# Kernel optimization log

Hardware: AMD Instinct MI355X
Metric: run time of the kernel (lower is better)

The kernel has to match this reference:

```python
import jax, jax.numpy as jnp
import numpy as np

B, S, E, H, D = 4, 2048, 1024, 16, 64  # batch, seq, embed, heads, head_dim


def setup_inputs() -> dict:
    key = jax.random.key(0)
    k1, k2, k3 = jax.random.split(key, 3)
    x = jax.random.normal(k1, (B, S, E), dtype=jnp.float32)
    qkv_w = jax.random.normal(k2, (E, H, 3 * D), dtype=jnp.float32) * (1.0 / np.sqrt(E))
    qkv_b = jnp.zeros((H, 3 * D), dtype=jnp.float32)
    out_w = jax.random.normal(k3, (H, D, E), dtype=jnp.float32) * (1.0 / np.sqrt(H * D))
    out_b = jnp.zeros((E,), dtype=jnp.float32)
    return {"x": x, "qkv_w": qkv_w, "qkv_b": qkv_b, "out_w": out_w, "out_b": out_b}


def _large_negative_number(dtype):
    return jnp.asarray(-0.7 * jnp.finfo(dtype).max, dtype=dtype)


def reference(x, qkv_w, qkv_b, out_w, out_b):
    # qkv projection: LinearGeneral(E -> (H, 3D))
    qkv = jnp.einsum('bse,ehd->bshd', x, qkv_w) + qkv_b  # [B,S,H,3D]
    q, k, v = jnp.split(qkv, 3, axis=-1)  # each [B,S,H,D]
    logits = jnp.einsum('bqhd,bkhd->bhqk', q, k)  # [B,H,S,S]
    logits = logits / jnp.sqrt(jnp.asarray(q.shape[-1], logits.dtype))
    mask = jnp.tril(jnp.ones((q.shape[1], q.shape[1]), dtype=jnp.bool_))
    logits = jnp.where(mask, logits, _large_negative_number(logits.dtype))
    probs = jax.nn.softmax(logits, axis=-1)
    attn = jnp.einsum('bhqk,bkhd->bqhd', probs, v)  # [B,S,H,D]
    # output projection: LinearGeneral((H, D) -> E)
    return jnp.einsum('bqhd,hde->bqe', attn, out_w) + out_b
```

## Files before the change

kernel.cpp:

```cpp
#include <hip/hip_runtime.h>

typedef unsigned int u32;
typedef _Float16 f16;
typedef _Float16 f16x8 __attribute__((ext_vector_type(8)));
typedef _Float16 f16x4 __attribute__((ext_vector_type(4)));
typedef float f32x4 __attribute__((ext_vector_type(4)));

#define LOG2E 1.4426950408889634f

__device__ __forceinline__ void gl_lds16(const void* g, void* l) {
  __builtin_amdgcn_global_load_lds(
      (const __attribute__((address_space(1))) u32*)g,
      (__attribute__((address_space(3))) u32*)l, 16, 0, 0);
}

__device__ __forceinline__ f32x4 mfma16(f16x8 a, f16x8 b, f32x4 c) {
  return __builtin_amdgcn_mfma_f32_16x16x32_f16(a, b, c, 0, 0, 0);
}

__global__ void k_cvt(const float* __restrict__ in, f16* __restrict__ out, int n8) {
  int stride = gridDim.x * blockDim.x;
  for (int i = blockIdx.x * blockDim.x + threadIdx.x; i < n8; i += stride) {
    f32x4 a = *(const f32x4*)(in + (size_t)i * 8);
    f32x4 b = *(const f32x4*)(in + (size_t)i * 8 + 4);
    f16x8 o;
    o[0] = (f16)a[0]; o[1] = (f16)a[1]; o[2] = (f16)a[2]; o[3] = (f16)a[3];
    o[4] = (f16)b[0]; o[5] = (f16)b[1]; o[6] = (f16)b[2]; o[7] = (f16)b[3];
    *(f16x8*)(out + (size_t)i * 8) = o;
  }
}

__global__ void k_tconv(const float* __restrict__ in, f16* __restrict__ out, int R, int C) {
  __shared__ f16 tile[32][33];
  int c0 = blockIdx.x * 32, r0 = blockIdx.y * 32;
  int tx = threadIdx.x, ty = threadIdx.y;
#pragma unroll
  for (int i = ty; i < 32; i += 8)
    tile[i][tx] = (f16)in[(size_t)(r0 + i) * C + c0 + tx];
  __syncthreads();
#pragma unroll
  for (int i = ty; i < 32; i += 8)
    out[(size_t)(c0 + i) * R + r0 + tx] = tile[tx][i];
}

__device__ __forceinline__ void gemm97(
    const f16* __restrict__ A, const f16* __restrict__ Bt,
    int bm, int bn, f16* SM, int w, int lane, f32x4 (&acc)[4][4]) {
  constexpr int KT = 32;
  const int g = lane >> 4, rl = lane & 15;
  const int l4 = lane >> 2, ls = lane & 3;
  const int sslot = ls ^ ((l4 >> 1) & 3);
  const int wr = w >> 1, wc = w & 1;

  const f16* aS = A + (size_t)(bm + w * 16 + l4) * 1024 + sslot * 8;
  const f16* bS = Bt + (size_t)(bn + w * 16 + l4) * 1024 + sslot * 8;

#define STG97(b, kt) do { \
    gl_lds16(aS + (kt) * 32,          SM + (b) * 8192 + w * 512); \
    gl_lds16(aS + 65536 + (kt) * 32,  SM + (b) * 8192 + 2048 + w * 512); \
    gl_lds16(bS + (kt) * 32,          SM + (b) * 8192 + 4096 + w * 512); \
    gl_lds16(bS + 65536 + (kt) * 32,  SM + (b) * 8192 + 6144 + w * 512); } while (0)

  const int ro = rl * 32 + ((g ^ ((rl >> 1) & 3)) * 8);

  STG97(0, 0);
  __syncthreads();

#pragma unroll 1
  for (int kt = 0; kt < KT; ++kt) {
    const int cur = kt & 1;
    if (kt + 1 < KT) STG97(cur ^ 1, kt + 1);
    const f16* SMb = SM + cur * 8192;
    f16x8 af[4], bf[4];
#pragma unroll
    for (int mi = 0; mi < 4; ++mi)
      af[mi] = *(const f16x8*)(SMb + wr * 2048 + mi * 512 + ro);
#pragma unroll
    for (int j = 0; j < 4; ++j)
      bf[j] = *(const f16x8*)(SMb + 4096 + wc * 2048 + j * 512 + ro);
    __builtin_amdgcn_s_setprio(1);
#pragma unroll
    for (int mi = 0; mi < 4; ++mi)
#pragma unroll
      for (int j = 0; j < 4; ++j)
        acc[mi][j] = mfma16(af[mi], bf[j], acc[mi][j]);
    __builtin_amdgcn_s_setprio(0);
    __syncthreads();
  }
#undef STG97
}

__global__ __launch_bounds__(256, 3) void k_gemm_qkv5(
    const f16* __restrict__ A, const f16* __restrict__ Bt,
    const float* __restrict__ bias,
    f16* __restrict__ qo, f16* __restrict__ ko2, f16* __restrict__ vto) {
  __shared__ __align__(16) f16 SM[16384];
  const int lin0 = blockIdx.y * 24 + blockIdx.x;
  const int lin = (lin0 & 7) * 192 + (lin0 >> 3);
  const int bn = (lin % 24) * 128, bm = (lin / 24) * 128;
  const int t = threadIdx.x, lane = t & 63, w = t >> 6;
  const int g = lane >> 4, rl = lane & 15;
  const int wr = w >> 1, wc = w & 1;

  f32x4 acc[4][4] = {};
  gemm97(A, Bt, bm, bn, SM, w, lane, acc);

#pragma unroll
  for (int i = 0; i < 4; ++i)
#pragma unroll
    for (int j = 0; j < 4; ++j)
#pragma unroll
      for (int r = 0; r < 4; ++r) {
        int m = bm + wr * 64 + i * 16 + g * 4 + r;
        int n = bn + wc * 64 + j * 16 + rl;
        float v = acc[i][j][r] + bias[n];
        int b = m >> 11, s = m & 2047;
        int h = n / 192, rem = n - h * 192;
        int tsel = rem >> 6, dd = rem & 63;
        size_t bh = (size_t)(b * 16 + h);
        if (tsel == 0)      qo[(bh * 2048 + s) * 64 + dd] = (f16)(v * (0.125f * LOG2E));
        else if (tsel == 1) ko2[(bh * 2048 + s) * 64 + dd] = (f16)v;
        else                vto[(bh * 64 + dd) * 2048 + s] = (f16)v;
      }
}

__global__ __launch_bounds__(256, 3) void k_gemm_out5(
    const f16* __restrict__ A, const f16* __restrict__ Bt,
    const float* __restrict__ bias, float* __restrict__ out) {
  __shared__ __align__(16) f16 SM[16384];
  const int lin0 = blockIdx.y * 8 + blockIdx.x;
  const int lin = (lin0 & 7) * 64 + (lin0 >> 3);
  const int bn = (lin % 8) * 128, bm = (lin / 8) * 128;
  const int t = threadIdx.x, lane = t & 63, w = t >> 6;
  const int g = lane >> 4, rl = lane & 15;
  const int wr = w >> 1, wc = w & 1;

  f32x4 acc[4][4] = {};
  gemm97(A, Bt, bm, bn, SM, w, lane, acc);

#pragma unroll
  for (int i = 0; i < 4; ++i)
#pragma unroll
    for (int j = 0; j < 4; ++j)
#pragma unroll
      for (int r = 0; r < 4; ++r) {
        int m = bm + wr * 64 + i * 16 + g * 4 + r;
        int n = bn + wc * 64 + j * 16 + rl;
        out[(size_t)m * 1024 + n] = acc[i][j][r] + bias[n];
      }
}

__global__ __launch_bounds__(256, 4) void k_attn5(
    const f16* __restrict__ q, const f16* __restrict__ kgl,
    const f16* __restrict__ vt, f16* __restrict__ o) {
  constexpr int S = 2048;
  __shared__ __align__(16) f16 Ks[2][64 * 64];
  __shared__ __align__(16) f16 Vs[2][64 * 64];
  __shared__ __align__(16) f16 Ps[4][16 * 64];

  const int d = blockIdx.x;
  const int bh = (d & 7) * 8 + ((d >> 3) & 7);
  const int v_ = d >> 6, g2 = v_ >> 2, r2 = v_ & 3;
  const int qb = (g2 == 0) ? 15 - r2 : (g2 == 1) ? r2 : (g2 == 2) ? 11 - r2 : 4 + r2;

  const int t = threadIdx.x, lane = t & 63, w = t >> 6;
  const int g = lane >> 4, rl = lane & 15;

  const f16* qp = q + ((size_t)bh * S + qb * 128) * 64;
  const f16* kb = kgl + (size_t)bh * S * 64;
  const f16* vb = vt + (size_t)bh * 64 * S;

  f16x8 qf[2][2];
#pragma unroll
  for (int sub = 0; sub < 2; ++sub)
#pragma unroll
    for (int ks = 0; ks < 2; ++ks)
      qf[sub][ks] = *(const f16x8*)(qp + (size_t)(w * 32 + sub * 16 + rl) * 64 + ks * 32 + g * 8);

  f32x4 oacc[2][4] = {};
  float lrow[2] = {0.f, 0.f};

  const int srow = lane >> 3;
  const int sslot = (lane & 7) ^ srow;

  const int nkt = 2 * qb + 2;
  const int qsub0 = qb * 128 + w * 32;
  const int qmaxw = qsub0 + 31;

  auto STAGE = [&](int bufi, int kt) {
#pragma unroll
    for (int i = 0; i < 2; ++i) {
      const int r0 = w * 16 + i * 8;
      gl_lds16(kb + (size_t)(kt * 64 + r0 + srow) * 64 + sslot * 8, &Ks[bufi][r0 * 64]);
      gl_lds16(vb + (size_t)(r0 + srow) * S + kt * 64 + sslot * 8, &Vs[bufi][r0 * 64]);
    }
  };

  STAGE(0, 0);
  __syncthreads();
  int buf = 0;

  for (int kt = 0; kt < nkt; ++kt) {
    if (kt + 1 < nkt) STAGE(buf ^ 1, kt + 1);

    if (kt * 64 <= qmaxw) {
      const f16* Kb = &Ks[buf][0];
      const f16* Vb = &Vs[buf][0];

      f32x4 sT[2][4] = {};
#pragma unroll
      for (int j = 0; j < 4; ++j)
#pragma unroll
        for (int ks = 0; ks < 2; ++ks) {
          int row = j * 16 + rl;
          f16x8 kf = *(const f16x8*)(Kb + row * 64 + (((ks * 4 + g) ^ (rl & 7)) * 8));
          sT[0][j] = mfma16(kf, qf[0][ks], sT[0][j]);
          sT[1][j] = mfma16(kf, qf[1][ks], sT[1][j]);
        }

      if (kt * 64 + 63 > qsub0) {
#pragma unroll
        for (int sub = 0; sub < 2; ++sub) {
          const int qs = qsub0 + sub * 16;
#pragma unroll
          for (int j = 0; j < 4; ++j)
#pragma unroll
            for (int r = 0; r < 4; ++r)
              if (kt * 64 + j * 16 + g * 4 + r > qs + rl) sT[sub][j][r] = -1e30f;
        }
      }

#pragma unroll
      for (int sub = 0; sub < 2; ++sub) {
        const int qsub = qsub0 + sub * 16;
        if (kt * 64 > qsub + 15) continue;

        float ps = 0.f;
#pragma unroll
        for (int j = 0; j < 4; ++j) {
          f16x4 pb;
#pragma unroll
          for (int r = 0; r < 4; ++r) {
            float pp = exp2f(sT[sub][j][r]);
            ps += pp;
            pb[r] = (f16)pp;
          }
          *(f16x4*)(&Ps[w][0] + rl * 64 + (((j * 2 + (g >> 1)) ^ (rl & 7)) * 8) + (g & 1) * 4) = pb;
        }
        lrow[sub] += ps;

        asm volatile("s_waitcnt lgkmcnt(0)" ::: "memory");
        __builtin_amdgcn_sched_barrier(0);

        f16x8 pf[2];
#pragma unroll
        for (int ks = 0; ks < 2; ++ks)
          pf[ks] = *(const f16x8*)(&Ps[w][0] + rl * 64 + (((ks * 4 + g) ^ (rl & 7)) * 8));

#pragma unroll
        for (int dj = 0; dj < 4; ++dj)
#pragma unroll
          for (int ks = 0; ks < 2; ++ks) {
            int vrow = dj * 16 + rl;
            f16x8 vf = *(const f16x8*)(Vb + vrow * 64 + (((ks * 4 + g) ^ (rl & 7)) * 8));
            oacc[sub][dj] = mfma16(pf[ks], vf, oacc[sub][dj]);
          }
      }
    }
    __syncthreads();
    buf ^= 1;
  }

  float rinv[2];
#pragma unroll
  for (int sub = 0; sub < 2; ++sub) {
    float s_ = lrow[sub];
    s_ += __shfl_xor(s_, 16, 64);
    s_ += __shfl_xor(s_, 32, 64);
    rinv[sub] = 1.0f / s_;
  }

  const int h = bh & 15;
  const size_t rowb = (size_t)(bh >> 4) * 2048 + qb * 128 + w * 32;
#pragma unroll
  for (int sub = 0; sub < 2; ++sub)
#pragma unroll
    for (int r = 0; r < 4; ++r) {
      float ri = __shfl(rinv[sub], g * 4 + r, 64);
#pragma unroll
      for (int dj = 0; dj < 4; ++dj)
        o[(rowb + sub * 16 + g * 4 + r) * 1024 + h * 64 + dj * 16 + rl] =
            (f16)(oacc[sub][dj][r] * ri);
    }
}

extern "C" void kernel_launch(void* const* d_in, const int* in_sizes, int n_in,
                              void* d_out, int out_size, void* d_ws, size_t ws_size,
                              hipStream_t stream) {
  (void)in_sizes; (void)n_in; (void)out_size; (void)ws_size;
  const float* x    = (const float*)d_in[0];
  const float* wqkv = (const float*)d_in[1];
  const float* bqkv = (const float*)d_in[2];
  const float* wo   = (const float*)d_in[3];
  const float* bo   = (const float*)d_in[4];
  float* out = (float*)d_out;
  char* ws = (char*)d_ws;

  f16* xb    = (f16*)(ws + 0);
  f16* wqkvt = (f16*)(ws + 16777216);
  f16* wot   = (f16*)(ws + 23068672);
  f16* qws   = (f16*)(ws + 25165824);
  f16* kws   = (f16*)(ws + 41943040);
  f16* vtws  = (f16*)(ws + 58720256);
  f16* attnb = xb;

  k_cvt<<<1024, 256, 0, stream>>>(x, xb, 8388608 / 8);
  k_tconv<<<dim3(96, 32), dim3(32, 8), 0, stream>>>(wqkv, wqkvt, 1024, 3072);
  k_tconv<<<dim3(32, 32), dim3(32, 8), 0, stream>>>(wo, wot, 1024, 1024);
  k_gemm_qkv5<<<dim3(24, 64), 256, 0, stream>>>(xb, wqkvt, bqkv, qws, kws, vtws);
  k_attn5<<<1024, 256, 0, stream>>>(qws, kws, vtws, attnb);
  k_gemm_out5<<<dim3(8, 64), 256, 0, stream>>>(attnb, wot, bo, out);
}
```

Baseline: 187.0 us.

## Use 128x256 triple-buffered QKV GEMM and restructure attention softmax/PV loop

Replaces the QKV projection GEMM with a 128x256 tile kernel. Each wave owns a 64-column slab with eight M fragments, fed by a three-stage LDS ring of async global-to-LDS loads with explicit waitcnt and barriers. In attention, the P·V MFMAs for both 16-row sub-tiles are merged into one loop that shares each V fragment load. MFMA sections run at raised wave priority, and exp results are packed with cvt_pkrtz. This trades higher LDS and register use (two blocks per CU instead of three) for more reuse per tile, and it drops the per-subtile causal skip in attention, which adds some wasted work on fully masked rows.

After: 184.1 us. Within noise of the previous version (-1.5%).

```diff
diff --git a/kernel.cpp b/kernel.cpp
--- a/kernel.cpp
+++ b/kernel.cpp
@@ -5,6 +5,7 @@
 typedef _Float16 f16x8 __attribute__((ext_vector_type(8)));
 typedef _Float16 f16x4 __attribute__((ext_vector_type(4)));
 typedef float f32x4 __attribute__((ext_vector_type(4)));
+typedef _Float16 __attribute__((address_space(3))) lf16;
 
 #define LOG2E 1.4426950408889634f
 
@@ -16,6 +17,12 @@
 
 __device__ __forceinline__ f32x4 mfma16(f16x8 a, f16x8 b, f32x4 c) {
   return __builtin_amdgcn_mfma_f32_16x16x32_f16(a, b, c, 0, 0, 0);
+}
+
+__device__ __forceinline__ f16x8 ldsr(const f16* p) {
+  f16x8 r;
+  asm volatile("ds_read_b128 %0, %1" : "=v"(r) : "v"((const lf16*)p));
+  return r;
 }
 
 __global__ void k_cvt(const float* __restrict__ in, f16* __restrict__ out, int n8) {
@@ -43,6 +50,124 @@
     out[(size_t)(c0 + i) * R + r0 + tx] = tile[tx][i];
 }
 
+__device__ __forceinline__ void gemm_fatA(
+    const f16* __restrict__ A, const f16* __restrict__ Bt,
+    int bm, int bn, f16* SM, int w, int lane, f32x4 (&acc)[8][4]) {
+  constexpr int KT = 32;
+  const int g = lane >> 4, rl = lane & 15;
+  const int l4 = lane >> 2, ls = lane & 3;
+  const int sslot = ls ^ ((l4 >> 1) & 3);
+
+  const f16* aS = A + (size_t)(bm + w * 32 + l4) * 1024 + sslot * 8;
+  const f16* bS = Bt + (size_t)(bn + w * 16 + l4) * 1024 + sslot * 8;
+  f16* aD = SM + w * 1024;
+  f16* bD = SM + 4096 + w * 512;
+
+#define ASTG0(b, kt) do { \
+    gl_lds16(aS + (kt) * 32,          aD + (b) * 12288); \
+    gl_lds16(aS + 16384 + (kt) * 32,  aD + (b) * 12288 + 512); \
+    gl_lds16(bS + (kt) * 32,          bD + (b) * 12288); } while (0)
+#define ASTG1(b, kt) do { \
+    gl_lds16(bS + 65536 + (kt) * 32,  bD + (b) * 12288 + 2048); \
+    gl_lds16(bS + 131072 + (kt) * 32, bD + (b) * 12288 + 4096); \
+    gl_lds16(bS + 196608 + (kt) * 32, bD + (b) * 12288 + 6144); } while (0)
+
+  ASTG0(0, 0); ASTG1(0, 0);
+  ASTG0(1, 1); ASTG1(1, 1);
+  asm volatile("s_waitcnt vmcnt(6)" ::: "memory");
+  __builtin_amdgcn_s_barrier();
+
+  const int ro = rl * 32 + ((g ^ ((rl >> 1) & 3)) * 8);
+
+  int c = 0, cs = 2;
+#pragma unroll 1
+  for (int kt = 0; kt < KT; ++kt) {
+    const f16* SMc = SM + c * 12288;
+    const bool stg = (kt + 2 < KT);
+    f16x8 bf[4], af[4];
+
+    {
+#pragma unroll
+      for (int j = 0; j < 4; ++j)
+        bf[j] = ldsr(SMc + 4096 + w * 2048 + j * 512 + ro);
+#pragma unroll
+      for (int mi = 0; mi < 4; ++mi)
+        af[mi] = ldsr(SMc + mi * 512 + ro);
+      if (stg) ASTG0(cs, kt + 2);
+      __builtin_amdgcn_s_barrier();
+      asm volatile("s_waitcnt lgkmcnt(0)");
+      __builtin_amdgcn_sched_barrier(0);
+      __builtin_amdgcn_s_setprio(1);
+#pragma unroll
+      for (int mi = 0; mi < 4; ++mi)
+#pragma unroll
+        for (int j = 0; j < 4; ++j)
+          acc[mi][j] = mfma16(af[mi], bf[j], acc[mi][j]);
+      __builtin_amdgcn_s_setprio(0);
+      __builtin_amdgcn_sched_barrier(0);
+      __builtin_amdgcn_s_barrier();
+    }
+    {
+#pragma unroll
+      for (int mi = 0; mi < 4; ++mi)
+        af[mi] = ldsr(SMc + (4 + mi) * 512 + ro);
+      if (stg) ASTG1(cs, kt + 2);
+      __builtin_amdgcn_s_barrier();
+      asm volatile("s_waitcnt lgkmcnt(0)");
+      __builtin_amdgcn_sched_barrier(0);
+      __builtin_amdgcn_s_setprio(1);
+#pragma unroll
+      for (int mi = 0; mi < 4; ++mi)
+#pragma unroll
+        for (int j = 0; j < 4; ++j)
+          acc[4 + mi][j] = mfma16(af[mi], bf[j], acc[4 + mi][j]);
+      __builtin_amdgcn_s_setprio(0);
+      __builtin_amdgcn_sched_barrier(0);
+      if (kt + 2 < KT)      { asm volatile("s_waitcnt vmcnt(6)" ::: "memory"); }
+      else if (kt + 1 < KT) { asm volatile("s_waitcnt vmcnt(0)" ::: "memory"); }
+      __builtin_amdgcn_s_barrier();
+      __builtin_amdgcn_sched_barrier(0);
+    }
+    c = (c == 2) ? 0 : c + 1;
+    cs = (cs == 2) ? 0 : cs + 1;
+  }
+#undef ASTG0
+#undef ASTG1
+}
+
+__global__ __launch_bounds__(256, 2) void k_gemm_qkv4(
+    const f16* __restrict__ A, const f16* __restrict__ Bt,
+    const float* __restrict__ bias,
+    f16* __restrict__ qo, f16* __restrict__ ko2, f16* __restrict__ vto) {
+  __shared__ __align__(16) f16 SM[36864];
+  const int lin0 = blockIdx.y * 12 + blockIdx.x;
+  const int lin = (lin0 & 7) * 96 + (lin0 >> 3);
+  const int bn = (lin % 12) * 256, bm = (lin / 12) * 128;
+  const int t = threadIdx.x, lane = t & 63, w = t >> 6;
+  const int g = lane >> 4, rl = lane & 15;
+
+  f32x4 acc[8][4] = {};
+  gemm_fatA(A, Bt, bm, bn, SM, w, lane, acc);
+
+#pragma unroll
+  for (int mi = 0; mi < 8; ++mi)
+#pragma unroll
+    for (int j = 0; j < 4; ++j)
+#pragma unroll
+      for (int r = 0; r < 4; ++r) {
+        int m = bm + mi * 16 + g * 4 + r;
+        int n = bn + w * 64 + j * 16 + rl;
+        float v = acc[mi][j][r] + bias[n];
+        int b = m >> 11, s = m & 2047;
+        int h = n / 192, rem = n - h * 192;
+        int tsel = rem >> 6, dd = rem & 63;
+        size_t bh = (size_t)(b * 16 + h);
+        if (tsel == 0)      qo[(bh * 2048 + s) * 64 + dd] = (f16)(v * (0.125f * LOG2E));
+        else if (tsel == 1) ko2[(bh * 2048 + s) * 64 + dd] = (f16)v;
+        else                vto[(bh * 64 + dd) * 2048 + s] = (f16)v;
+      }
+}
+
 __device__ __forceinline__ void gemm97(
     const f16* __restrict__ A, const f16* __restrict__ Bt,
     int bm, int bn, f16* SM, int w, int lane, f32x4 (&acc)[4][4]) {
@@ -88,40 +213,6 @@
     __syncthreads();
   }
 #undef STG97
-}
-
-__global__ __launch_bounds__(256, 3) void k_gemm_qkv5(
-    const f16* __restrict__ A, const f16* __restrict__ Bt,
-    const float* __restrict__ bias,
-    f16* __restrict__ qo, f16* __restrict__ ko2, f16* __restrict__ vto) {
-  __shared__ __align__(16) f16 SM[16384];
-  const int lin0 = blockIdx.y * 24 + blockIdx.x;
-  const int lin = (lin0 & 7) * 192 + (lin0 >> 3);
-  const int bn = (lin % 24) * 128, bm = (lin / 24) * 128;
-  const int t = threadIdx.x, lane = t & 63, w = t >> 6;
-  const int g = lane >> 4, rl = lane & 15;
-  const int wr = w >> 1, wc = w & 1;
-
-  f32x4 acc[4][4] = {};
-  gemm97(A, Bt, bm, bn, SM, w, lane, acc);
-
-#pragma unroll
-  for (int i = 0; i < 4; ++i)
-#pragma unroll
-    for (int j = 0; j < 4; ++j)
-#pragma unroll
-      for (int r = 0; r < 4; ++r) {
-        int m = bm + wr * 64 + i * 16 + g * 4 + r;
-        int n = bn + wc * 64 + j * 16 + rl;
-        float v = acc[i][j][r] + bias[n];
-        int b = m >> 11, s = m & 2047;
-        int h = n / 192, rem = n - h * 192;
-        int tsel = rem >> 6, dd = rem & 63;
-        size_t bh = (size_t)(b * 16 + h);
-        if (tsel == 0)      qo[(bh * 2048 + s) * 64 + dd] = (f16)(v * (0.125f * LOG2E));
-        else if (tsel == 1) ko2[(bh * 2048 + s) * 64 + dd] = (f16)v;
-        else                vto[(bh * 64 + dd) * 2048 + s] = (f16)v;
-      }
 }
 
 __global__ __launch_bounds__(256, 3) void k_gemm_out5(
@@ -150,7 +241,7 @@
       }
 }
 
-__global__ __launch_bounds__(256, 4) void k_attn5(
+__global__ __launch_bounds__(256, 4) void k_attn6(
     const f16* __restrict__ q, const f16* __restrict__ kgl,
     const f16* __restrict__ vt, f16* __restrict__ o) {
   constexpr int S = 2048;
@@ -208,6 +299,7 @@
       const f16* Vb = &Vs[buf][0];
 
       f32x4 sT[2][4] = {};
+      __builtin_amdgcn_s_setprio(1);
 #pragma unroll
       for (int j = 0; j < 4; ++j)
 #pragma unroll
@@ -217,6 +309,7 @@
           sT[0][j] = mfma16(kf, qf[0][ks], sT[0][j]);
           sT[1][j] = mfma16(kf, qf[1][ks], sT[1][j]);
         }
+      __builtin_amdgcn_s_setprio(0);
 
       if (kt * 64 + 63 > qsub0) {
 #pragma unroll
@@ -230,21 +323,21 @@
         }
       }
 
+      f16x8 pf[2][2];
 #pragma unroll
       for (int sub = 0; sub < 2; ++sub) {
-        const int qsub = qsub0 + sub * 16;
-        if (kt * 64 > qsub + 15) continue;
-
         float ps = 0.f;
 #pragma unroll
         for (int j = 0; j < 4; ++j) {
+          float p0 = exp2f(sT[sub][j][0]);
+          float p1 = exp2f(sT[sub][j][1]);
+          float p2 = exp2f(sT[sub][j][2]);
+          float p3 = exp2f(sT[sub][j][3]);
+          ps += (p0 + p1) + (p2 + p3);
+          auto lo = __builtin_amdgcn_cvt_pkrtz(p0, p1);
+          auto hi = __builtin_amdgcn_cvt_pkrtz(p2, p3);
           f16x4 pb;
-#pragma unroll
-          for (int r = 0; r < 4; ++r) {
-            float pp = exp2f(sT[sub][j][r]);
-            ps += pp;
-            pb[r] = (f16)pp;
-          }
+          pb[0] = (f16)lo[0]; pb[1] = (f16)lo[1]; pb[2] = (f16)hi[0]; pb[3] = (f16)hi[1];
           *(f16x4*)(&Ps[w][0] + rl * 64 + (((j * 2 + (g >> 1)) ^ (rl & 7)) * 8) + (g & 1) * 4) = pb;
         }
         lrow[sub] += ps;
@@ -252,20 +345,22 @@
         asm volatile("s_waitcnt lgkmcnt(0)" ::: "memory");
         __builtin_amdgcn_sched_barrier(0);
 
-        f16x8 pf[2];
 #pragma unroll
         for (int ks = 0; ks < 2; ++ks)
-          pf[ks] = *(const f16x8*)(&Ps[w][0] + rl * 64 + (((ks * 4 + g) ^ (rl & 7)) * 8));
-
-#pragma unroll
-        for (int dj = 0; dj < 4; ++dj)
-#pragma unroll
-          for (int ks = 0; ks < 2; ++ks) {
-            int vrow = dj * 16 + rl;
-            f16x8 vf = *(const f16x8*)(Vb + vrow * 64 + (((ks * 4 + g) ^ (rl & 7)) * 8));
-            oacc[sub][dj] = mfma16(pf[ks], vf, oacc[sub][dj]);
-          }
+          pf[sub][ks] = *(const f16x8*)(&Ps[w][0] + rl * 64 + (((ks * 4 + g) ^ (rl & 7)) * 8));
       }
+
+      __builtin_amdgcn_s_setprio(1);
+#pragma unroll
+      for (int dj = 0; dj < 4; ++dj)
+#pragma unroll
+        for (int ks = 0; ks < 2; ++ks) {
+          int vrow = dj * 16 + rl;
+          f16x8 vf = *(const f16x8*)(Vb + vrow * 64 + (((ks * 4 + g) ^ (rl & 7)) * 8));
+          oacc[0][dj] = mfma16(pf[0][ks], vf, oacc[0][dj]);
+          oacc[1][dj] = mfma16(pf[1][ks], vf, oacc[1][dj]);
+        }
+      __builtin_amdgcn_s_setprio(0);
     }
     __syncthreads();
     buf ^= 1;
@@ -317,7 +412,7 @@
   k_cvt<<<1024, 256, 0, stream>>>(x, xb, 8388608 / 8);
   k_tconv<<<dim3(96, 32), dim3(32, 8), 0, stream>>>(wqkv, wqkvt, 1024, 3072);
   k_tconv<<<dim3(32, 32), dim3(32, 8), 0, stream>>>(wo, wot, 1024, 1024);
-  k_gemm_qkv5<<<dim3(24, 64), 256, 0, stream>>>(xb, wqkvt, bqkv, qws, kws, vtws);
-  k_attn5<<<1024, 256, 0, stream>>>(qws, kws, vtws, attnb);
+  k_gemm_qkv4<<<dim3(12, 64), 256, 0, stream>>>(xb, wqkvt, bqkv, qws, kws, vtws);
+  k_attn6<<<1024, 256, 0, stream>>>(qws, kws, vtws, attnb);
   k_gemm_out5<<<dim3(8, 64), 256, 0, stream>>>(attnb, wot, bo, out);
 }
```
